# Kernel tuning notes

Measured on AMD Instinct MI355X. Metric: run time of the kernel, lower is better.

The kernel has to match this reference:

```python
import jax, jax.numpy as jnp
import numpy as np


def setup_inputs() -> dict:
    key = jax.random.key(0)
    k1, k2 = jax.random.split(key)
    n, c, h, w = 4, 64, 128, 128
    x = jax.random.normal(k1, (n, c, h, w), dtype=jnp.float32)
    # weight holds 9 stencil taps per channel, layout matches F.unfold: (n, c*9, h, w)
    weight = jax.random.normal(k2, (n, c * 9, h, w), dtype=jnp.float32)
    return {"x": x, "weight": weight, "max_step": 8}


def reference(x, weight, max_step):
    n, c, h, w = x.shape
    # normalize |w| over the 9 taps (done once, outside the loop, as in the original)
    wgt = jnp.abs(weight.reshape(n, c, 9, h, w))
    wgt = wgt / jnp.sum(wgt, axis=2, keepdims=True)

    steps = min(max_step, max(h, w))  # static Python ints -> static trip count

    def step(xx, _):
        # 3x3 patches via 9 shifted views of the padded image; tap order k = ki*3 + kj
        # matches F.unfold's row-major kernel ordering.
        xp = jnp.pad(xx, ((0, 0), (0, 0), (1, 1), (1, 1)))
        patches = jnp.stack(
            [xp[:, :, i:i + h, j:j + w] for i in range(3) for j in range(3)],
            axis=2,
        )  # (n, c, 9, h, w)
        return jnp.sum(patches * wgt, axis=2), None

    x_out, _ = jax.lax.scan(step, x, None, length=steps)
    return x_out
```

## Files before the change

kernel.cpp:

```cpp
#include <hip/hip_runtime.h>
#include <hip/hip_fp16.h>


constexpr int H = 128, W = 128, PLANE = H * W;
constexpr int NSTEP = 8;
constexpr int RPT  = 3;
constexpr int NRG  = 16;
constexpr int HALO = 8;
constexpr int OWN  = 32;

#define MKWIN(D, V) do {                                                     \
    (D)[1] = (V).x; (D)[2] = (V).y; (D)[3] = (V).z; (D)[4] = (V).w;          \
    float _l = __shfl_up((V).w, 1);                                          \
    float _r = __shfl_down((V).x, 1);                                        \
    (D)[0] = (quad == 0)  ? 0.f : _l;                                        \
    (D)[5] = (quad == 31) ? 0.f : _r;                                        \
} while (0)

__global__ __launch_bounds__(512)
void diff_fused(const float* __restrict__ xin,
                const float* __restrict__ wgt,
                float* __restrict__ out)
{
    __shared__ float ldsT[NRG][W];
    __shared__ float ldsB[NRG][W];

    const int tid   = threadIdx.x;
    const int quad  = tid & 31;
    const int rg    = tid >> 5;
    const int j0    = quad * 4;
    const int plane = blockIdx.x >> 2;
    const int qtr   = blockIdx.x & 3;
    const int rbase = qtr * OWN - HALO;
    const int r0    = rbase + rg * RPT;
    const size_t pbase = (size_t)plane * PLANE;

    const float* __restrict__ xp = xin + pbase;
    const float* __restrict__ wb = wgt + pbase * 9;

    __half2 wh[RPT][9][2];
    #pragma unroll
    for (int p = 0; p < RPT; ++p) {
        const int  gr  = r0 + p;
        const bool inr = (unsigned)gr < (unsigned)H;
        const float* wr = wb + gr * W + j0;
        float a[9][4];
        float s0 = 0.f, s1 = 0.f, s2 = 0.f, s3 = 0.f;
        #pragma unroll
        for (int k = 0; k < 9; ++k) {
            float4 v = make_float4(1.f, 1.f, 1.f, 1.f);
            if (inr) v = *reinterpret_cast<const float4*>(wr + (size_t)k * PLANE);
            a[k][0] = fabsf(v.x); a[k][1] = fabsf(v.y);
            a[k][2] = fabsf(v.z); a[k][3] = fabsf(v.w);
            s0 += a[k][0]; s1 += a[k][1]; s2 += a[k][2]; s3 += a[k][3];
        }
        s0 = 1.f / s0; s1 = 1.f / s1; s2 = 1.f / s2; s3 = 1.f / s3;
        #pragma unroll
        for (int k = 0; k < 9; ++k) {
            wh[p][k][0] = __halves2half2(__float2half_rn(a[k][0] * s0),
                                         __float2half_rn(a[k][1] * s1));
            wh[p][k][1] = __halves2half2(__float2half_rn(a[k][2] * s2),
                                         __float2half_rn(a[k][3] * s3));
        }
    }

    float4 xr[RPT];
    #pragma unroll
    for (int p = 0; p < RPT; ++p) {
        const int gr = r0 + p;
        xr[p] = make_float4(0.f, 0.f, 0.f, 0.f);
        if ((unsigned)gr < (unsigned)H)
            xr[p] = *reinterpret_cast<const float4*>(xp + gr * W + j0);
    }

    #pragma unroll 1
    for (int s = 0; s < NSTEP; ++s) {
        *reinterpret_cast<float4*>(&ldsT[rg][j0]) = xr[0];
        *reinterpret_cast<float4*>(&ldsB[rg][j0]) = xr[RPT - 1];
        __syncthreads();
        float4 up = make_float4(0.f, 0.f, 0.f, 0.f);
        float4 dn = make_float4(0.f, 0.f, 0.f, 0.f);
        if (rg > 0)       up = *reinterpret_cast<const float4*>(&ldsB[rg - 1][j0]);
        if (rg < NRG - 1) dn = *reinterpret_cast<const float4*>(&ldsT[rg + 1][j0]);
        __syncthreads();

        float win[3][6];
        MKWIN(win[0], up);
        MKWIN(win[1], xr[0]);
        #pragma unroll
        for (int p = 0; p < RPT; ++p) {
            if (p < RPT - 1) { MKWIN(win[(p + 2) % 3], xr[p + 1]); }
            else             { MKWIN(win[(p + 2) % 3], dn); }
            float a0 = 0.f, a1 = 0.f, a2 = 0.f, a3 = 0.f;
            #pragma unroll
            for (int di = 0; di < 3; ++di) {
                #pragma unroll
                for (int dj = 0; dj < 3; ++dj) {
                    const int k = di * 3 + dj;
                    const __half2 w0 = wh[p][k][0];
                    const __half2 w1 = wh[p][k][1];
                    a0 = fmaf(__low2float (w0), win[(p + di) % 3][dj + 0], a0);
                    a1 = fmaf(__high2float(w0), win[(p + di) % 3][dj + 1], a1);
                    a2 = fmaf(__low2float (w1), win[(p + di) % 3][dj + 2], a2);
                    a3 = fmaf(__high2float(w1), win[(p + di) % 3][dj + 3], a3);
                }
            }
            xr[p] = make_float4(a0, a1, a2, a3);
        }
        #pragma unroll
        for (int p = 0; p < RPT; ++p) {
            const int gr = r0 + p;
            if ((unsigned)gr >= (unsigned)H)
                xr[p] = make_float4(0.f, 0.f, 0.f, 0.f);
        }
    }

    float* __restrict__ op = out + pbase;
    #pragma unroll
    for (int p = 0; p < RPT; ++p) {
        const int gr = r0 + p;
        const int lr = gr - rbase - HALO;
        if ((unsigned)lr < (unsigned)OWN)
            *reinterpret_cast<float4*>(op + gr * W + j0) = xr[p];
    }
}

extern "C" void kernel_launch(void* const* d_in, const int* in_sizes, int n_in,
                              void* d_out, int out_size, void* d_ws, size_t ws_size,
                              hipStream_t stream)
{
    const float* x = (const float*)d_in[0];
    const float* w = (const float*)d_in[1];
    float* out = (float*)d_out;
    (void)d_ws; (void)ws_size; (void)in_sizes; (void)n_in; (void)out_size;

    diff_fused<<<dim3(4 * 4 * 64), dim3(512), 0, stream>>>(x, w, out);
}
```

Baseline: 287.1 us.

## Process whole plane per 1024-thread block, dropping halo recompute

Each block now covers an entire 128x128 plane with 1024 threads (32 row-groups of 4 rows), instead of four 512-thread blocks per plane that each recomputed an 8-row halo. This removes redundant weight loads and halo computation plus the boundary masking. The weight loads are also reordered to issue all rows of a tap together, with normalization applied afterwards. The grid shrinks to 256 blocks, so fewer blocks are available to fill the GPU's compute units, and register pressure rises under a 1024-thread launch bound.

```diff
diff --git a/kernel.cpp b/kernel.cpp
--- a/kernel.cpp
+++ b/kernel.cpp
@@ -4,10 +4,8 @@
 
 constexpr int H = 128, W = 128, PLANE = H * W;
 constexpr int NSTEP = 8;
-constexpr int RPT  = 3;
-constexpr int NRG  = 16;
-constexpr int HALO = 8;
-constexpr int OWN  = 32;
+constexpr int RPT  = 4;
+constexpr int NRG  = 32;
 
 #define MKWIN(D, V) do {                                                     \
     (D)[1] = (V).x; (D)[2] = (V).y; (D)[3] = (V).z; (D)[4] = (V).w;          \
@@ -17,7 +15,7 @@
     (D)[5] = (quad == 31) ? 0.f : _r;                                        \
 } while (0)
 
-__global__ __launch_bounds__(512)
+__global__ __launch_bounds__(1024)
 void diff_fused(const float* __restrict__ xin,
                 const float* __restrict__ wgt,
                 float* __restrict__ out)
@@ -29,52 +27,55 @@
     const int quad  = tid & 31;
     const int rg    = tid >> 5;
     const int j0    = quad * 4;
-    const int plane = blockIdx.x >> 2;
-    const int qtr   = blockIdx.x & 3;
-    const int rbase = qtr * OWN - HALO;
-    const int r0    = rbase + rg * RPT;
-    const size_t pbase = (size_t)plane * PLANE;
+    const int r0    = rg * RPT;
+    const size_t pbase = (size_t)blockIdx.x * PLANE;
 
     const float* __restrict__ xp = xin + pbase;
     const float* __restrict__ wb = wgt + pbase * 9;
 
     __half2 wh[RPT][9][2];
+    float s[RPT][4];
+    #pragma unroll
+    for (int p = 0; p < RPT; ++p) { s[p][0] = s[p][1] = s[p][2] = s[p][3] = 0.f; }
+
+    #pragma unroll
+    for (int k = 0; k < 9; ++k) {
+        const float* wk = wb + (size_t)k * PLANE + r0 * W + j0;
+        float4 v[RPT];
+        #pragma unroll
+        for (int p = 0; p < RPT; ++p)
+            v[p] = *reinterpret_cast<const float4*>(wk + p * W);
+        #pragma unroll
+        for (int p = 0; p < RPT; ++p) {
+            const float a0 = fabsf(v[p].x), a1 = fabsf(v[p].y);
+            const float a2 = fabsf(v[p].z), a3 = fabsf(v[p].w);
+            s[p][0] += a0; s[p][1] += a1; s[p][2] += a2; s[p][3] += a3;
+            wh[p][k][0] = __halves2half2(__float2half_rn(a0), __float2half_rn(a1));
+            wh[p][k][1] = __halves2half2(__float2half_rn(a2), __float2half_rn(a3));
+        }
+    }
     #pragma unroll
     for (int p = 0; p < RPT; ++p) {
-        const int  gr  = r0 + p;
-        const bool inr = (unsigned)gr < (unsigned)H;
-        const float* wr = wb + gr * W + j0;
-        float a[9][4];
-        float s0 = 0.f, s1 = 0.f, s2 = 0.f, s3 = 0.f;
+        const float i0 = 1.f / s[p][0], i1 = 1.f / s[p][1];
+        const float i2 = 1.f / s[p][2], i3 = 1.f / s[p][3];
         #pragma unroll
         for (int k = 0; k < 9; ++k) {
-            float4 v = make_float4(1.f, 1.f, 1.f, 1.f);
-            if (inr) v = *reinterpret_cast<const float4*>(wr + (size_t)k * PLANE);
-            a[k][0] = fabsf(v.x); a[k][1] = fabsf(v.y);
-            a[k][2] = fabsf(v.z); a[k][3] = fabsf(v.w);
-            s0 += a[k][0]; s1 += a[k][1]; s2 += a[k][2]; s3 += a[k][3];
-        }
-        s0 = 1.f / s0; s1 = 1.f / s1; s2 = 1.f / s2; s3 = 1.f / s3;
-        #pragma unroll
-        for (int k = 0; k < 9; ++k) {
-            wh[p][k][0] = __halves2half2(__float2half_rn(a[k][0] * s0),
-                                         __float2half_rn(a[k][1] * s1));
-            wh[p][k][1] = __halves2half2(__float2half_rn(a[k][2] * s2),
-                                         __float2half_rn(a[k][3] * s3));
+            wh[p][k][0] = __halves2half2(
+                __float2half_rn(__low2float (wh[p][k][0]) * i0),
+                __float2half_rn(__high2float(wh[p][k][0]) * i1));
+            wh[p][k][1] = __halves2half2(
+                __float2half_rn(__low2float (wh[p][k][1]) * i2),
+                __float2half_rn(__high2float(wh[p][k][1]) * i3));
         }
     }
 
     float4 xr[RPT];
     #pragma unroll
-    for (int p = 0; p < RPT; ++p) {
-        const int gr = r0 + p;
-        xr[p] = make_float4(0.f, 0.f, 0.f, 0.f);
-        if ((unsigned)gr < (unsigned)H)
-            xr[p] = *reinterpret_cast<const float4*>(xp + gr * W + j0);
-    }
+    for (int p = 0; p < RPT; ++p)
+        xr[p] = *reinterpret_cast<const float4*>(xp + (r0 + p) * W + j0);
 
     #pragma unroll 1
-    for (int s = 0; s < NSTEP; ++s) {
+    for (int st = 0; st < NSTEP; ++st) {
         *reinterpret_cast<float4*>(&ldsT[rg][j0]) = xr[0];
         *reinterpret_cast<float4*>(&ldsB[rg][j0]) = xr[RPT - 1];
         __syncthreads();
@@ -107,22 +108,12 @@
             }
             xr[p] = make_float4(a0, a1, a2, a3);
         }
-        #pragma unroll
-        for (int p = 0; p < RPT; ++p) {
-            const int gr = r0 + p;
-            if ((unsigned)gr >= (unsigned)H)
-                xr[p] = make_float4(0.f, 0.f, 0.f, 0.f);
-        }
     }
 
     float* __restrict__ op = out + pbase;
     #pragma unroll
-    for (int p = 0; p < RPT; ++p) {
-        const int gr = r0 + p;
-        const int lr = gr - rbase - HALO;
-        if ((unsigned)lr < (unsigned)OWN)
-            *reinterpret_cast<float4*>(op + gr * W + j0) = xr[p];
-    }
+    for (int p = 0; p < RPT; ++p)
+        *reinterpret_cast<float4*>(op + (r0 + p) * W + j0) = xr[p];
 }
 
 extern "C" void kernel_launch(void* const* d_in, const int* in_sizes, int n_in,
@@ -134,5 +125,5 @@
     float* out = (float*)d_out;
     (void)d_ws; (void)ws_size; (void)in_sizes; (void)n_in; (void)out_size;
 
-    diff_fused<<<dim3(4 * 4 * 64), dim3(512), 0, stream>>>(x, w, out);
+    diff_fused<<<dim3(4 * 64), dim3(1024), 0, stream>>>(x, w, out);
 }
```

Result: slower. 378.4 us (+31.8%).
